# Kernel optimization log

Measured on AMD Instinct MI355X. Metric: run time of the kernel, lower is better.

The kernel has to match this reference:

```python
import jax, jax.numpy as jnp
import numpy as np

BN_EPS = 1e-5

def setup_inputs() -> dict:
    key = jax.random.key(0)
    k1, k2 = jax.random.split(key)
    B, C, H, W, K = 256, 2048, 7, 7, 16
    featmap = jax.random.normal(k1, (B, C, H, W), dtype=jnp.float32)
    w16 = jax.random.normal(k2, (K, C), dtype=jnp.float32) * 0.02  # 1x1 conv weight
    bn_gamma = jnp.ones((K,), jnp.float32)
    bn_beta = jnp.zeros((K,), jnp.float32)
    bn_mean = jnp.zeros((K,), jnp.float32)
    bn_var = jnp.ones((K,), jnp.float32)
    return {"featmap": featmap, "w16": w16, "bn_gamma": bn_gamma,
            "bn_beta": bn_beta, "bn_mean": bn_mean, "bn_var": bn_var}

def reference(featmap, w16, bn_gamma, bn_beta, bn_mean, bn_var):
    # featmap: [B, 2048, 7, 7]; 1x1 conv -> featcov16: [B, 16, 7, 7]
    featcov16 = jnp.einsum('bchw,kc->bkhw', featmap, w16)
    # BatchNorm2d(16), inference-style with running stats
    inv = bn_gamma / jnp.sqrt(bn_var + BN_EPS)
    featcov16 = featcov16 * inv[None, :, None, None] + (bn_beta - bn_mean * inv)[None, :, None, None]
    # Loop-free bilinear pooling: original repeats featcov16[:,i] to 2048 ch,
    # multiplies with featmap, and AvgPool2d(7) -> mean over HxW.
    HW = featmap.shape[2] * featmap.shape[3]
    feat_matrix = jnp.einsum('bkhw,bchw->bkc', featcov16, featmap) / HW  # [B,16,2048]
    bp_out_feat = feat_matrix.reshape(feat_matrix.shape[0], -1)  # [B, 32768]
    return bp_out_feat
```

## Files before the change

### kernel.cpp

```cpp
#include <hip/hip_runtime.h>

#define BATCH 256
#define CDIM  2048
#define HW    49
#define KDIM  16

#define OSTRIP 8
#define SC     256
#define STRIP_B (SC * HW * 4)
#define NLOAD  (STRIP_B / 1024)

#define GLDS(g, l) __builtin_amdgcn_global_load_lds(                        \
        (const __attribute__((address_space(1))) unsigned int*)(g),          \
        (__attribute__((address_space(3))) unsigned int*)(l), 16, 0, 0)


__global__ __launch_bounds__(256) void prep_kernel(
    const float* __restrict__ w16,
    const float* __restrict__ gamma, const float* __restrict__ var,
    float* __restrict__ wT)
{
    const int idx = blockIdx.x * 256 + threadIdx.x;
    const int c = idx >> 4, k = idx & 15;
    const float inv = gamma[k] * rsqrtf(var[k] + 1e-5f) * (1.0f / 49.0f);
    wT[idx] = w16[k * CDIM + c] * inv;
}

__global__ __launch_bounds__(256) void conv_kernel(
    const float* __restrict__ fm, const float* __restrict__ wT,
    float* __restrict__ pscr)
{
    __shared__ __align__(16) float fbuf[SC * HW + 4];
    __shared__ __align__(16) float red[4 * KDIM * 52];

    const int tid  = threadIdx.x;
    const int b    = blockIdx.x >> 3;
    const int o    = blockIdx.x & 7;
    const int wavu = __builtin_amdgcn_readfirstlane(tid >> 6);
    const int lane = tid & 63;
    const int hwi  = lane < HW ? lane : HW - 1;

    {
        const char* gbase = (const char*)fm
            + (size_t)b * (CDIM * HW * 4) + (size_t)o * STRIP_B;
        char* lbase = (char*)fbuf;
        const int nld = (wavu == 0) ? 13 : 12;
        for (int i = 0; i < nld; ++i) {
            const int j = wavu + 4 * i;
            GLDS(gbase + j * 1024 + lane * 16, lbase + j * 1024);
        }
    }
    __syncthreads();

    float acc[KDIM];
    #pragma unroll
    for (int k = 0; k < KDIM; ++k) acc[k] = 0.f;

    const int cl0 = wavu * 64;
    const float4* __restrict__ wq = (const float4*)(wT + (size_t)((o * SC + cl0) << 4));

    #pragma unroll 8
    for (int cc = 0; cc < 64; ++cc) {
        const float fv = fbuf[(cl0 + cc) * HW + hwi];
        const float4 w0 = wq[cc * 4 + 0];
        const float4 w1 = wq[cc * 4 + 1];
        const float4 w2 = wq[cc * 4 + 2];
        const float4 w3 = wq[cc * 4 + 3];
        acc[0]  += w0.x * fv; acc[1]  += w0.y * fv; acc[2]  += w0.z * fv; acc[3]  += w0.w * fv;
        acc[4]  += w1.x * fv; acc[5]  += w1.y * fv; acc[6]  += w1.z * fv; acc[7]  += w1.w * fv;
        acc[8]  += w2.x * fv; acc[9]  += w2.y * fv; acc[10] += w2.z * fv; acc[11] += w2.w * fv;
        acc[12] += w3.x * fv; acc[13] += w3.y * fv; acc[14] += w3.z * fv; acc[15] += w3.w * fv;
    }

    if (lane < HW) {
        #pragma unroll
        for (int k = 0; k < KDIM; ++k)
            red[wavu * (KDIM * 52) + k * 52 + lane] = acc[k];
    }
    __syncthreads();
    for (int p = tid; p < HW * KDIM; p += 256) {
        const int k = p / HW, hw = p - k * HW;
        const int a = k * 52 + hw;
        const float s = red[a] + red[a + 832] + red[a + 1664] + red[a + 2496];
        pscr[(size_t)blockIdx.x * 784 + p] = s;
    }
}

__global__ __launch_bounds__(256) void mid_kernel(
    float* __restrict__ pscr,
    const float* __restrict__ gamma, const float* __restrict__ beta,
    const float* __restrict__ mean,  const float* __restrict__ var)
{
    const int tid  = threadIdx.x;
    const size_t base = (size_t)blockIdx.x * (OSTRIP * 784);
    float s0 = 0.f, s1 = 0.f, s2 = 0.f, s3 = 0.f;

#define MIDR(SV, R) { const int j = tid + 256 * (R); if (j < 784) {            \
        const int k = j & 15, hw = j >> 4;                                     \
        const size_t src = base + k * HW + hw;                                 \
        float t = 0.f;                                                         \
        _Pragma("unroll")                                                      \
        for (int oo = 0; oo < OSTRIP; ++oo) t += pscr[src + oo * 784];         \
        const float inv = gamma[k] * rsqrtf(var[k] + 1e-5f);                   \
        SV = t + (beta[k] - mean[k] * inv) * (1.0f / 49.0f); } }
    MIDR(s0, 0) MIDR(s1, 1) MIDR(s2, 2) MIDR(s3, 3)
#undef MIDR
    __syncthreads();
    if (tid < 784)        pscr[base + tid]       = s0;
    if (tid + 256 < 784)  pscr[base + tid + 256] = s1;
    if (tid + 512 < 784)  pscr[base + tid + 512] = s2;
    if (tid + 768 < 784)  pscr[base + tid + 768] = s3;
}

__global__ __launch_bounds__(256) void bp_kernel(
    const float* __restrict__ fm, const float* __restrict__ pscr,
    float* __restrict__ out)
{
    __shared__ __align__(16) float fs[256 * HW];

    const int tid = threadIdx.x;
    const int b   = blockIdx.x >> 3;
    const int oc  = (blockIdx.x & 7) * 256;

    {
        const float4* src = (const float4*)(fm + ((size_t)b * CDIM + oc) * HW);
        float4* dst = (float4*)fs;
        for (int i = tid; i < (256 * HW) / 4; i += 256) dst[i] = src[i];
    }
    __syncthreads();

    const float4* __restrict__ P4 = (const float4*)(pscr + (size_t)b * (OSTRIP * 784));

    float acc[KDIM];
    #pragma unroll
    for (int k = 0; k < KDIM; ++k) acc[k] = 0.f;

    const float* row = fs + tid * HW;
    #pragma unroll
    for (int hw = 0; hw < HW; ++hw) {
        const float fv = row[hw];
        const float4 p0 = P4[hw * 4 + 0];
        const float4 p1 = P4[hw * 4 + 1];
        const float4 p2 = P4[hw * 4 + 2];
        const float4 p3 = P4[hw * 4 + 3];
        acc[0]  += p0.x * fv; acc[1]  += p0.y * fv; acc[2]  += p0.z * fv; acc[3]  += p0.w * fv;
        acc[4]  += p1.x * fv; acc[5]  += p1.y * fv; acc[6]  += p1.z * fv; acc[7]  += p1.w * fv;
        acc[8]  += p2.x * fv; acc[9]  += p2.y * fv; acc[10] += p2.z * fv; acc[11] += p2.w * fv;
        acc[12] += p3.x * fv; acc[13] += p3.y * fv; acc[14] += p3.z * fv; acc[15] += p3.w * fv;
    }

    float* ob = out + (size_t)b * (KDIM * CDIM) + oc + tid;
    #pragma unroll
    for (int k = 0; k < KDIM; ++k) ob[k * CDIM] = acc[k];
}

extern "C" void kernel_launch(void* const* d_in, const int* in_sizes, int n_in,
                              void* d_out, int out_size, void* d_ws, size_t ws_size,
                              hipStream_t stream) {
    const float* fm    = (const float*)d_in[0];
    const float* w16   = (const float*)d_in[1];
    const float* gamma = (const float*)d_in[2];
    const float* beta  = (const float*)d_in[3];
    const float* mean  = (const float*)d_in[4];
    const float* var   = (const float*)d_in[5];
    float* out  = (float*)d_out;
    float* wT   = (float*)d_ws;
    float* pscr = (float*)d_ws + CDIM * KDIM;

    prep_kernel<<<128, 256, 0, stream>>>(w16, gamma, var, wT);
    conv_kernel<<<BATCH * OSTRIP, 256, 0, stream>>>(fm, wT, pscr);
    mid_kernel<<<BATCH, 256, 0, stream>>>(pscr, gamma, beta, mean, var);
    bp_kernel<<<BATCH * 8, 256, 0, stream>>>(fm, pscr, out);
}
```

Baseline: 220.5 us.

## Fuse strip reduction into conv via atomics, drop mid kernel, use LDS-direct loads in bp

The separate mid_kernel reduction is removed. prep_kernel now initializes the per-batch scratch with the BN bias term, and conv_kernel atomically adds its strip partial sums into a compact [B,49,16] buffer. The reduction buffer reuses the feature LDS, which lowers shared memory use and may raise occupancy. bp_kernel now loads its feature tile with global_load_lds instead of float4 copies through registers. This saves a launch and a scratch round trip, at the cost of float atomic contention (8 adders per address) and nondeterministic summation order.

After: 250.3 us. 1.13x slower.

```diff
diff --git a/kernel.cpp b/kernel.cpp
--- a/kernel.cpp
+++ b/kernel.cpp
@@ -8,7 +8,6 @@
 #define OSTRIP 8
 #define SC     256
 #define STRIP_B (SC * HW * 4)
-#define NLOAD  (STRIP_B / 1024)
 
 #define GLDS(g, l) __builtin_amdgcn_global_load_lds(                        \
         (const __attribute__((address_space(1))) unsigned int*)(g),          \
@@ -17,13 +16,20 @@
 
 __global__ __launch_bounds__(256) void prep_kernel(
     const float* __restrict__ w16,
-    const float* __restrict__ gamma, const float* __restrict__ var,
-    float* __restrict__ wT)
+    const float* __restrict__ gamma, const float* __restrict__ beta,
+    const float* __restrict__ mean,  const float* __restrict__ var,
+    float* __restrict__ wT, float* __restrict__ pscr)
 {
     const int idx = blockIdx.x * 256 + threadIdx.x;
     const int c = idx >> 4, k = idx & 15;
     const float inv = gamma[k] * rsqrtf(var[k] + 1e-5f) * (1.0f / 49.0f);
     wT[idx] = w16[k * CDIM + c] * inv;
+
+    for (int i = idx; i < BATCH * (HW * KDIM); i += 128 * 256) {
+        const int kk = i & 15;
+        const float invk = gamma[kk] * rsqrtf(var[kk] + 1e-5f);
+        pscr[i] = (beta[kk] - mean[kk] * invk) * (1.0f / 49.0f);
+    }
 }
 
 __global__ __launch_bounds__(256) void conv_kernel(
@@ -31,7 +37,6 @@
     float* __restrict__ pscr)
 {
     __shared__ __align__(16) float fbuf[SC * HW + 4];
-    __shared__ __align__(16) float red[4 * KDIM * 52];
 
     const int tid  = threadIdx.x;
     const int b    = blockIdx.x >> 3;
@@ -72,64 +77,47 @@
         acc[12] += w3.x * fv; acc[13] += w3.y * fv; acc[14] += w3.z * fv; acc[15] += w3.w * fv;
     }
 
+    __syncthreads();
+    float* red = fbuf;
     if (lane < HW) {
         #pragma unroll
         for (int k = 0; k < KDIM; ++k)
             red[wavu * (KDIM * 52) + k * 52 + lane] = acc[k];
     }
     __syncthreads();
+
     for (int p = tid; p < HW * KDIM; p += 256) {
         const int k = p / HW, hw = p - k * HW;
         const int a = k * 52 + hw;
         const float s = red[a] + red[a + 832] + red[a + 1664] + red[a + 2496];
-        pscr[(size_t)blockIdx.x * 784 + p] = s;
+        atomicAdd(&pscr[(size_t)b * 784 + hw * KDIM + k], s);
     }
-}
-
-__global__ __launch_bounds__(256) void mid_kernel(
-    float* __restrict__ pscr,
-    const float* __restrict__ gamma, const float* __restrict__ beta,
-    const float* __restrict__ mean,  const float* __restrict__ var)
-{
-    const int tid  = threadIdx.x;
-    const size_t base = (size_t)blockIdx.x * (OSTRIP * 784);
-    float s0 = 0.f, s1 = 0.f, s2 = 0.f, s3 = 0.f;
-
-#define MIDR(SV, R) { const int j = tid + 256 * (R); if (j < 784) {            \
-        const int k = j & 15, hw = j >> 4;                                     \
-        const size_t src = base + k * HW + hw;                                 \
-        float t = 0.f;                                                         \
-        _Pragma("unroll")                                                      \
-        for (int oo = 0; oo < OSTRIP; ++oo) t += pscr[src + oo * 784];         \
-        const float inv = gamma[k] * rsqrtf(var[k] + 1e-5f);                   \
-        SV = t + (beta[k] - mean[k] * inv) * (1.0f / 49.0f); } }
-    MIDR(s0, 0) MIDR(s1, 1) MIDR(s2, 2) MIDR(s3, 3)
-#undef MIDR
-    __syncthreads();
-    if (tid < 784)        pscr[base + tid]       = s0;
-    if (tid + 256 < 784)  pscr[base + tid + 256] = s1;
-    if (tid + 512 < 784)  pscr[base + tid + 512] = s2;
-    if (tid + 768 < 784)  pscr[base + tid + 768] = s3;
 }
 
 __global__ __launch_bounds__(256) void bp_kernel(
     const float* __restrict__ fm, const float* __restrict__ pscr,
     float* __restrict__ out)
 {
-    __shared__ __align__(16) float fs[256 * HW];
+    __shared__ __align__(16) float fs[SC * HW];
 
-    const int tid = threadIdx.x;
-    const int b   = blockIdx.x >> 3;
-    const int oc  = (blockIdx.x & 7) * 256;
+    const int tid  = threadIdx.x;
+    const int b    = blockIdx.x >> 3;
+    const int oc   = (blockIdx.x & 7) * SC;
+    const int wavu = __builtin_amdgcn_readfirstlane(tid >> 6);
+    const int lane = tid & 63;
 
     {
-        const float4* src = (const float4*)(fm + ((size_t)b * CDIM + oc) * HW);
-        float4* dst = (float4*)fs;
-        for (int i = tid; i < (256 * HW) / 4; i += 256) dst[i] = src[i];
+        const char* gbase = (const char*)fm + ((size_t)b * CDIM + oc) * (HW * 4);
+        char* lbase = (char*)fs;
+        const int nld = (wavu == 0) ? 13 : 12;
+        for (int i = 0; i < nld; ++i) {
+            const int j = wavu + 4 * i;
+            GLDS(gbase + j * 1024 + lane * 16, lbase + j * 1024);
+        }
     }
     __syncthreads();
 
-    const float4* __restrict__ P4 = (const float4*)(pscr + (size_t)b * (OSTRIP * 784));
+    const float4* __restrict__ P4 = (const float4*)(pscr + (size_t)b * 784);
 
     float acc[KDIM];
     #pragma unroll
@@ -167,8 +155,7 @@
     float* wT   = (float*)d_ws;
     float* pscr = (float*)d_ws + CDIM * KDIM;
 
-    prep_kernel<<<128, 256, 0, stream>>>(w16, gamma, var, wT);
+    prep_kernel<<<128, 256, 0, stream>>>(w16, gamma, beta, mean, var, wT, pscr);
     conv_kernel<<<BATCH * OSTRIP, 256, 0, stream>>>(fm, wT, pscr);
-    mid_kernel<<<BATCH, 256, 0, stream>>>(pscr, gamma, beta, mean, var);
-    bp_kernel<<<BATCH * 8, 256, 0, stream>>>(fm, pscr, out);
+    bp_kernel<<<BATCH * OSTRIP, 256, 0, stream>>>(fm, pscr, out);
 }
```
